# Performance work log

Hardware: AMD Instinct MI355X
Metric: run time of the kernel (lower is better)

Reference implementation:

```python
import jax, jax.numpy as jnp
import numpy as np

N = 50000      # num_nodes
E = 800000     # num_edges
D = 128        # hidden_dim
POOL_RATIO = 0.5
CROSS_W = 1.0  # cross_weight


def _gcn(x, W, b, src, dst, n):
    """GCNConv: symmetric-normalized aggregation with self-loops. Dropout is identity (eval)."""
    loops = jnp.arange(n)
    s = jnp.concatenate([src, loops])
    d = jnp.concatenate([dst, loops])
    deg = jax.ops.segment_sum(jnp.ones(s.shape, x.dtype), d, num_segments=n)
    inv_sqrt = jax.lax.rsqrt(jnp.maximum(deg, 1.0))  # deg >= 1 due to self-loops
    xw = x @ W                                        # [n, D]
    msg = xw[s] * (inv_sqrt[s] * inv_sqrt[d])[:, None]  # [E+n, D] gather
    return jax.ops.segment_sum(msg, d, num_segments=n) + b


def _prelu(x, a):
    return jnp.where(x >= 0, x, a * x)


def setup_inputs() -> dict:
    key = jax.random.key(0)
    ks = jax.random.split(key, 8)
    glorot = lambda k, sh: jax.random.normal(k, sh, jnp.float32) * np.float32(np.sqrt(2.0 / (sh[0] + sh[1])))
    return {
        "feat": jax.random.normal(ks[0], (N, D), jnp.float32),
        "h_neg": jax.random.normal(ks[1], (N, D), jnp.float32),
        "edge_index": jax.random.randint(ks[2], (2, E), 0, N),
        "Wd": glorot(ks[3], (D, D)),
        "bd": jnp.zeros((D,), jnp.float32),
        "prelu_a": jnp.full((1,), 0.25, jnp.float32),
        "Wbil": glorot(ks[4], (D, D)),
        "bbil": jnp.zeros((1,), jnp.float32),
        "Wg1": glorot(ks[5], (D, D)),
        "bg1": jnp.zeros((D,), jnp.float32),
        "Wg2": glorot(ks[6], (D, D)),
        "bg2": jnp.zeros((D,), jnp.float32),
        "Wg3": glorot(ks[7], (D, D)),
        "bg3": jnp.zeros((D,), jnp.float32),
    }


def reference(feat, h_neg, edge_index, Wd, bd, prelu_a, Wbil, bbil,
              Wg1, bg1, Wg2, bg2, Wg3, bg3):
    src, dst = edge_index[0], edge_index[1]
    # --- IndexSelect: dense layer on pos/neg features ---
    h_pos = _prelu(feat @ Wd + bd, prelu_a)
    h_neg_d = _prelu(h_neg @ Wd + bd, prelu_a)
    embed = _gcn(h_pos, Wg1, bg1, src, dst, N)
    h_center = jax.nn.sigmoid(embed)
    # Discriminator (bilinear) positive scores -> node importance
    score_pos = jnp.einsum('nd,de,ne->n', h_pos, Wbil, h_center) + bbil[0]
    _ = jnp.einsum('nd,de,ne->n', h_neg_d, Wbil, h_center) + bbil[0]  # score_neg (logits branch)
    scores = jax.nn.sigmoid(score_pos)
    order = jnp.argsort(-scores)           # descending
    k = int(POOL_RATIO * N)
    select_idx = order[:k]
    select_scores = scores[order][:k]
    # --- GraphPool (use_gcn=True): down-sample GCN, gather, scale ---
    pooled = _gcn(embed, Wg2, bg2, src, dst, N)[select_idx] * select_scores[:, None]
    # --- GraphUnpool: scatter into zeros, up-sample GCN ---
    fine = jnp.zeros((N, D), feat.dtype).at[select_idx].set(pooled)
    out = _gcn(fine, Wg3, bg3, src, dst, N)
    # --- cross/fuse connection ---
    return out + CROSS_W * embed
```

## Files before the change

### kernel.cpp

```cpp
#include <hip/hip_runtime.h>
#include <hip/hip_bf16.h>

#define NN 50000
#define NE 800000
#define DD 128
#define KSEL 25000
#define NBK 391
#define NBLKA 98

typedef unsigned int uint32;
typedef unsigned short ushort16;

__device__ __forceinline__ float sigmoidf(float x){ return 1.f/(1.f+__expf(-x)); }

__device__ __forceinline__ unsigned short f2b(float f){
  union{float f; unsigned u;} v; v.f=f;
  unsigned r=(v.u + 0x7fffu + ((v.u>>16)&1u))>>16;
  return (unsigned short)r;
}

__device__ __forceinline__ void addbf2(float&lo,float&hi,uint32 u,float w){
  lo+=__uint_as_float(u<<16)*w;
  hi+=__uint_as_float(u&0xffff0000u)*w;
}

__global__ __launch_bounds__(1024) void k_bcount(const int* __restrict__ dst,
    int* __restrict__ btot, int* __restrict__ blkcnt){
  __shared__ int h[NBK];
  int tid=threadIdx.x;
  for(int i=tid;i<NBK;i+=1024) h[i]=0;
  __syncthreads();
  int e0=blockIdx.x*8192;
  #pragma unroll
  for(int t=0;t<8;t++){
    int e=e0+t*1024+tid;
    if(e<NE) atomicAdd(&h[dst[e]>>7],1);
  }
  __syncthreads();
  for(int i=tid;i<NBK;i+=1024){
    int c=h[i];
    blkcnt[blockIdx.x*NBK+i]=c;
    if(c) atomicAdd(&btot[i],c);
  }
}

__global__ __launch_bounds__(512) void k_bscan(const int* __restrict__ btot,
    int* __restrict__ boff, const int* __restrict__ blkcnt, int* __restrict__ blkbase,
    int* __restrict__ row_start){
  __shared__ int sdata[512];
  int tid=threadIdx.x;
  int v=(tid<NBK)?btot[tid]:0;
  sdata[tid]=v; __syncthreads();
  for(int off=1;off<512;off<<=1){
    int y=(tid>=off)?sdata[tid-off]:0;
    __syncthreads();
    sdata[tid]+=y;
    __syncthreads();
  }
  int excl=sdata[tid]-v;
  if(tid<NBK) boff[tid]=excl;
  if(tid==NBK-1){ boff[NBK]=excl+v; row_start[NN]=NE; }
  if(tid<NBK){
    int run=excl;
    for(int b=0;b<NBLKA;b++){
      int c=blkcnt[b*NBK+tid];
      blkbase[b*NBK+tid]=run;
      run+=c;
    }
  }
}

__global__ __launch_bounds__(1024) void k_bscatter(const int* __restrict__ src,
    const int* __restrict__ dst, const int* __restrict__ blkbase, uint32* __restrict__ pairs){
  __shared__ int cur[NBK];
  int tid=threadIdx.x;
  for(int i=tid;i<NBK;i+=1024) cur[i]=blkbase[blockIdx.x*NBK+i];
  __syncthreads();
  int e0=blockIdx.x*8192;
  #pragma unroll
  for(int t=0;t<8;t++){
    int e=e0+t*1024+tid;
    if(e<NE){
      int d=dst[e];
      int p=atomicAdd(&cur[d>>7],1);
      pairs[p]=(unsigned)src[e] | ((unsigned)(d&127)<<17);
    }
  }
}

__global__ __launch_bounds__(256) void k_bfinal(const uint32* __restrict__ pairs,
    const int* __restrict__ boff, int* __restrict__ row_start,
    float* __restrict__ inv_sq, int* __restrict__ csr_src){
  __shared__ int degl[128];
  __shared__ int cur[128];
  __shared__ int ssum[2];
  int b=blockIdx.x, tid=threadIdx.x;
  int lo=boff[b], hi=boff[b+1];
  if(tid<128) degl[tid]=0;
  __syncthreads();
  for(int e=lo+tid;e<hi;e+=256) atomicAdd(&degl[pairs[e]>>17],1);
  __syncthreads();
  int v=0,x=0;
  if(tid<128){
    v=degl[tid]; x=v;
    #pragma unroll
    for(int off=1;off<64;off<<=1){
      int y=__shfl_up(x,off,64);
      if((tid&63)>=off) x+=y;
    }
    if((tid&63)==63) ssum[tid>>6]=x;
  }
  __syncthreads();
  if(tid<128){
    int incl=x+((tid>=64)?ssum[0]:0);
    int node=b*128+tid;
    int excl=lo+incl-v;
    if(node<NN){
      row_start[node]=excl;
      cur[tid]=excl;
      inv_sq[node]=1.f/sqrtf((float)(v+1));
    }
  }
  __syncthreads();
  for(int e=lo+tid;e<hi;e+=256){
    uint32 u=pairs[e];
    int p=atomicAdd(&cur[u>>17],1);
    csr_src[p]=(int)(u&0x1FFFFu);
  }
}

__global__ void k_transpose(const float* __restrict__ W, float* __restrict__ Wt){
  int idx=blockIdx.x*256+threadIdx.x;
  if(idx<DD*DD){
    int k=idx>>7, c=idx&127;
    Wt[idx]=W[c*DD+k];
  }
}

template<int IN_SIG,int ACT,int OUT_BF16,int FUSE_SCORE,int ROWLIST>
__global__ __launch_bounds__(256) void k_gemm96(const float* __restrict__ A,
    const float* __restrict__ W, const float* __restrict__ bias,
    float* __restrict__ outf, ushort16* __restrict__ outb,
    const float* __restrict__ aparam, const float* __restrict__ hp,
    const float* __restrict__ bbil, float* __restrict__ score,
    const int* __restrict__ rlist){
  __shared__ float Al[96][132];
  int tid=threadIdx.x;
  int row0=blockIdx.x*96;
  {
    #pragma unroll
    for(int i=0;i<12;i++){
      int idx=i*256+tid;
      int r=idx>>5, c=(idx&31)*4;
      int gr; bool ok;
      if(ROWLIST){ int ri=row0+r; ok=(ri<KSEL); gr=ok?rlist[ri]:0; }
      else { gr=row0+r; ok=(gr<NN); }
      float4 v=make_float4(0.f,0.f,0.f,0.f);
      if(ok) v=*(const float4*)&A[(size_t)gr*DD+c];
      if(IN_SIG){ v.x=sigmoidf(v.x); v.y=sigmoidf(v.y); v.z=sigmoidf(v.z); v.w=sigmoidf(v.w); }
      *(float4*)&Al[r][c]=v;
    }
  }
  __syncthreads();
  int tx=tid&15, ty=tid>>4;
  float acc[6][8];
  #pragma unroll
  for(int i=0;i<6;i++)
    #pragma unroll
    for(int c=0;c<8;c++) acc[i][c]=0.f;

  for(int k=0;k<DD;k+=4){
    float wv[4][8];
    #pragma unroll
    for(int r=0;r<4;r++){
      float4 lo=*(const float4*)&W[(size_t)(k+r)*DD+tx*8];
      float4 hi=*(const float4*)&W[(size_t)(k+r)*DD+tx*8+4];
      wv[r][0]=lo.x; wv[r][1]=lo.y; wv[r][2]=lo.z; wv[r][3]=lo.w;
      wv[r][4]=hi.x; wv[r][5]=hi.y; wv[r][6]=hi.z; wv[r][7]=hi.w;
    }
    #pragma unroll
    for(int i=0;i<6;i++){
      float4 a=*(const float4*)&Al[ty+16*i][k];
      #pragma unroll
      for(int c=0;c<8;c++)
        acc[i][c]+=a.x*wv[0][c]+a.y*wv[1][c]+a.z*wv[2][c]+a.w*wv[3][c];
    }
  }

  if(FUSE_SCORE){
    float bb=bbil[0];
    #pragma unroll
    for(int i=0;i<6;i++){
      int r=row0+ty+16*i;
      float p=0.f;
      if(r<NN){
        float4 h0=*(const float4*)&hp[(size_t)r*DD+tx*8];
        float4 h1=*(const float4*)&hp[(size_t)r*DD+tx*8+4];
        p=acc[i][0]*h0.x+acc[i][1]*h0.y+acc[i][2]*h0.z+acc[i][3]*h0.w
         +acc[i][4]*h1.x+acc[i][5]*h1.y+acc[i][6]*h1.z+acc[i][7]*h1.w;
      }
      p+=__shfl_xor(p,1,64); p+=__shfl_xor(p,2,64);
      p+=__shfl_xor(p,4,64); p+=__shfl_xor(p,8,64);
      if(tx==0 && r<NN) score[r]=sigmoidf(p+bb);
    }
    return;
  }
  float bl[8]={0,0,0,0,0,0,0,0};
  if(bias){
    float4 b0=*(const float4*)&bias[tx*8];
    float4 b1=*(const float4*)&bias[tx*8+4];
    bl[0]=b0.x; bl[1]=b0.y; bl[2]=b0.z; bl[3]=b0.w;
    bl[4]=b1.x; bl[5]=b1.y; bl[6]=b1.z; bl[7]=b1.w;
  }
  float ap=ACT?aparam[0]:0.f;
  #pragma unroll
  for(int i=0;i<6;i++){
    int ri=row0+ty+16*i;
    int r; bool ok;
    if(ROWLIST){ ok=(ri<KSEL); r=ok?rlist[ri]:0; }
    else { r=ri; ok=(r<NN); }
    if(ok){
      float o[8];
      #pragma unroll
      for(int c=0;c<8;c++){
        float t=acc[i][c]+bl[c];
        if(ACT) t=t>=0.f?t:ap*t;
        o[c]=t;
      }
      if(OUT_BF16){
        uint4 pk;
        pk.x=((uint32)f2b(o[1])<<16)|f2b(o[0]);
        pk.y=((uint32)f2b(o[3])<<16)|f2b(o[2]);
        pk.z=((uint32)f2b(o[5])<<16)|f2b(o[4]);
        pk.w=((uint32)f2b(o[7])<<16)|f2b(o[6]);
        *(uint4*)&outb[(size_t)r*DD+tx*8]=pk;
      } else {
        float4 q0; q0.x=o[0]; q0.y=o[1]; q0.z=o[2]; q0.w=o[3];
        float4 q1; q1.x=o[4]; q1.y=o[5]; q1.z=o[6]; q1.w=o[7];
        *(float4*)&outf[(size_t)r*DD+tx*8]=q0;
        *(float4*)&outf[(size_t)r*DD+tx*8+4]=q1;
      }
    }
  }
}

__global__ __launch_bounds__(256) void k_agg_f32(const float* __restrict__ xw,
    const int* __restrict__ row_start, const int* __restrict__ csr,
    const float* __restrict__ inv, const float* __restrict__ bias,
    float* __restrict__ outp){
  int node=blockIdx.x*4+(threadIdx.x>>6);
  if(node>=NN) return;
  int lane=threadIdx.x&63;
  int g=lane>>5, li=lane&31;
  int rs=row_start[node], re=row_start[node+1];
  float a0=0.f,a1=0.f,a2=0.f,a3=0.f;
  int j=rs;
  for(; j+7<re; j+=8){
    int s0=csr[j+g], s1=csr[j+2+g], s2=csr[j+4+g], s3=csr[j+6+g];
    float w0=inv[s0], w1=inv[s1], w2=inv[s2], w3=inv[s3];
    float4 v0=*(const float4*)&xw[(size_t)s0*DD+li*4];
    float4 v1=*(const float4*)&xw[(size_t)s1*DD+li*4];
    float4 v2=*(const float4*)&xw[(size_t)s2*DD+li*4];
    float4 v3=*(const float4*)&xw[(size_t)s3*DD+li*4];
    a0+=v0.x*w0+v1.x*w1+v2.x*w2+v3.x*w3;
    a1+=v0.y*w0+v1.y*w1+v2.y*w2+v3.y*w3;
    a2+=v0.z*w0+v1.z*w1+v2.z*w2+v3.z*w3;
    a3+=v0.w*w0+v1.w*w1+v2.w*w2+v3.w*w3;
  }
  for(; j+1<re; j+=2){
    int s=csr[j+g];
    float w=inv[s];
    float4 v=*(const float4*)&xw[(size_t)s*DD+li*4];
    a0+=v.x*w; a1+=v.y*w; a2+=v.z*w; a3+=v.w*w;
  }
  if(j<re && g==0){
    int s=csr[j]; float w=inv[s];
    float4 v=*(const float4*)&xw[(size_t)s*DD+li*4];
    a0+=v.x*w; a1+=v.y*w; a2+=v.z*w; a3+=v.w*w;
  }
  if(g==0){
    float wd=inv[node];
    float4 v=*(const float4*)&xw[(size_t)node*DD+li*4];
    a0+=v.x*wd; a1+=v.y*wd; a2+=v.z*wd; a3+=v.w*wd;
  }
  a0+=__shfl_xor(a0,32,64); a1+=__shfl_xor(a1,32,64);
  a2+=__shfl_xor(a2,32,64); a3+=__shfl_xor(a3,32,64);
  if(g==0){
    float wn=inv[node];
    float4 bv=*(const float4*)&bias[li*4];
    float4 o;
    o.x=a0*wn+bv.x; o.y=a1*wn+bv.y; o.z=a2*wn+bv.z; o.w=a3*wn+bv.w;
    *(float4*)&outp[(size_t)node*DD+li*4]=o;
  }
}

template<int MODE>
__global__ __launch_bounds__(256) void k_agg_b16(const uint32* __restrict__ xwb,
    const int* __restrict__ row_start, const int* __restrict__ csr,
    const float* __restrict__ inv, const float* __restrict__ bias,
    float* __restrict__ outp, const float* __restrict__ score,
    const unsigned char* __restrict__ sel, const float* __restrict__ addbuf,
    const int* __restrict__ list){
  int idx4=blockIdx.x*4+(threadIdx.x>>6);
  int node;
  if(MODE==1){ if(idx4>=KSEL) return; node=list[idx4]; }
  else { node=idx4; if(node>=NN) return; }
  int lane=threadIdx.x&63;
  int g=lane>>4, li=lane&15;
  int rs=row_start[node], re=row_start[node+1];
  float a[8];
  #pragma unroll
  for(int c=0;c<8;c++) a[c]=0.f;
  int j=rs;
  for(; j+7<re; j+=8){
    int sA=csr[j+g], sB=csr[j+4+g];
    if(MODE!=2 || sel[sA]){
      float w=inv[sA];
      uint4 u=*(const uint4*)(xwb+(size_t)sA*64+li*4);
      addbf2(a[0],a[1],u.x,w); addbf2(a[2],a[3],u.y,w);
      addbf2(a[4],a[5],u.z,w); addbf2(a[6],a[7],u.w,w);
    }
    if(MODE!=2 || sel[sB]){
      float w=inv[sB];
      uint4 u=*(const uint4*)(xwb+(size_t)sB*64+li*4);
      addbf2(a[0],a[1],u.x,w); addbf2(a[2],a[3],u.y,w);
      addbf2(a[4],a[5],u.z,w); addbf2(a[6],a[7],u.w,w);
    }
  }
  for(; j+3<re; j+=4){
    int s=csr[j+g];
    if(MODE!=2 || sel[s]){
      float w=inv[s];
      uint4 u=*(const uint4*)(xwb+(size_t)s*64+li*4);
      addbf2(a[0],a[1],u.x,w); addbf2(a[2],a[3],u.y,w);
      addbf2(a[4],a[5],u.z,w); addbf2(a[6],a[7],u.w,w);
    }
  }
  int rem=re-j;
  if(g<rem){
    int s=csr[j+g];
    if(MODE!=2 || sel[s]){
      float w=inv[s];
      uint4 u=*(const uint4*)(xwb+(size_t)s*64+li*4);
      addbf2(a[0],a[1],u.x,w); addbf2(a[2],a[3],u.y,w);
      addbf2(a[4],a[5],u.z,w); addbf2(a[6],a[7],u.w,w);
    }
  }
  if(g==0 && (MODE!=2 || sel[node])){
    float wd=inv[node];
    uint4 u=*(const uint4*)(xwb+(size_t)node*64+li*4);
    addbf2(a[0],a[1],u.x,wd); addbf2(a[2],a[3],u.y,wd);
    addbf2(a[4],a[5],u.z,wd); addbf2(a[6],a[7],u.w,wd);
  }
  #pragma unroll
  for(int c=0;c<8;c++){
    a[c]+=__shfl_xor(a[c],16,64);
    a[c]+=__shfl_xor(a[c],32,64);
  }
  if(g<2){
    float wn=inv[node];
    int cb=li*8+g*4;
    float4 bv=*(const float4*)&bias[cb];
    float r0=a[g*4+0]*wn+bv.x, r1=a[g*4+1]*wn+bv.y;
    float r2=a[g*4+2]*wn+bv.z, r3=a[g*4+3]*wn+bv.w;
    if(MODE==1){
      float sc=score[node];
      r0*=sc; r1*=sc; r2*=sc; r3*=sc;
    } else {
      float4 ad=*(const float4*)&addbuf[(size_t)node*DD+cb];
      r0+=ad.x; r1+=ad.y; r2+=ad.z; r3+=ad.w;
    }
    float4 o; o.x=r0; o.y=r1; o.z=r2; o.w=r3;
    *(float4*)&outp[(size_t)node*DD+cb]=o;
  }
}

template<int NB,int PASS>
__global__ __launch_bounds__(256) void k_hist(const float* __restrict__ score,
    int* __restrict__ ghist, const int* __restrict__ ctrl){
  __shared__ int lh[NB];
  int tid=threadIdx.x;
  for(int i=tid;i<NB;i+=256) lh[i]=0;
  __syncthreads();
  int p0=0,p01=0;
  if(PASS==1) p0=ctrl[0];
  if(PASS==2) p01=ctrl[2];
  for(int i=blockIdx.x*256+tid; i<NN; i+=gridDim.x*256){
    unsigned b=__float_as_uint(score[i]);
    if(PASS==0) atomicAdd(&lh[b>>20],1);
    else if(PASS==1){ if((int)(b>>20)==p0) atomicAdd(&lh[(b>>8)&0xFFF],1); }
    else { if((int)(b>>8)==p01) atomicAdd(&lh[b&0xFF],1); }
  }
  __syncthreads();
  for(int i=tid;i<NB;i+=256){ int v=lh[i]; if(v) atomicAdd(&ghist[i],v); }
}

template<int NB,int PASS>
__global__ void k_findb(const int* __restrict__ hist, int* __restrict__ ctrl){
  const int NT=NB/4;
  __shared__ int gsum[NT];
  int t=threadIdx.x;
  int s=hist[t*4]+hist[t*4+1]+hist[t*4+2]+hist[t*4+3];
  int x=s; gsum[t]=x; __syncthreads();
  for(int off=1;off<NT;off<<=1){
    int y=(t+off<NT)?gsum[t+off]:0;
    __syncthreads();
    x+=y; gsum[t]=x; __syncthreads();
  }
  int base;
  if(PASS==0) base=0; else if(PASS==1) base=ctrl[1]; else base=ctrl[3];
  int above=base+((t<NT-1)?gsum[t+1]:0);
  int incl=base+gsum[t];
  if(above<KSEL && incl>=KSEL){
    int c=above, B=0;
    for(int b=3;b>=0;b--){
      int hb=hist[t*4+b];
      if(c+hb>=KSEL){ B=t*4+b; break; }
      c+=hb;
    }
    if(PASS==0){ ctrl[0]=B; ctrl[1]=c; }
    else if(PASS==1){ ctrl[2]=(ctrl[0]<<12)|B; ctrl[3]=c; }
    else { ctrl[4]=(int)((((unsigned)ctrl[2])<<8)|(unsigned)B); ctrl[5]=KSEL-c; }
  }
}

__global__ void k_sel(const float* __restrict__ score, int* __restrict__ ctrl,
                      int* __restrict__ tie_list, unsigned char* __restrict__ sel,
                      int* __restrict__ list){
  int i=blockIdx.x*256+threadIdx.x;
  if(i>=NN) return;
  unsigned b=__float_as_uint(score[i]);
  unsigned thr=(unsigned)ctrl[4];
  if(b>thr){
    sel[i]=1;
    int p=atomicAdd(&ctrl[7],1);
    list[p]=i;
  }
  else if(b==thr){
    sel[i]=0;
    int p=atomicAdd(&ctrl[6],1);
    if(p<4096) tie_list[p]=i;
  } else sel[i]=0;
}

__global__ __launch_bounds__(256) void k_tie(const int* __restrict__ ctrl_c,
    int* __restrict__ ctrl, const int* __restrict__ tie_list,
    unsigned char* __restrict__ sel, int* __restrict__ list){
  int m=ctrl_c[6]; if(m>4096) m=4096;
  int needed=ctrl_c[5];
  for(int t=threadIdx.x; t<m; t+=blockDim.x){
    int idx=tie_list[t];
    int rank=0;
    for(int j=0;j<m;j++) rank+=(tie_list[j]<idx)?1:0;
    if(rank<needed){
      sel[idx]=1;
      int p=atomicAdd(&ctrl[7],1);
      list[p]=idx;
    }
  }
}

extern "C" void kernel_launch(void* const* d_in, const int* in_sizes, int n_in,
                              void* d_out, int out_size, void* d_ws, size_t ws_size,
                              hipStream_t stream){
  const float* feat   =(const float*)d_in[0];
  const int*   ei     =(const int*)  d_in[2];
  const int*   src    = ei;
  const int*   dst    = ei + NE;
  const float* Wd     =(const float*)d_in[3];
  const float* bd     =(const float*)d_in[4];
  const float* prelu_a=(const float*)d_in[5];
  const float* Wbil   =(const float*)d_in[6];
  const float* bbil   =(const float*)d_in[7];
  const float* Wg1    =(const float*)d_in[8];
  const float* bg1    =(const float*)d_in[9];
  const float* Wg2    =(const float*)d_in[10];
  const float* bg2    =(const float*)d_in[11];
  const float* Wg3    =(const float*)d_in[12];
  const float* bg3    =(const float*)d_in[13];
  float* out=(float*)d_out;

  char* p=(char*)d_ws;
  auto alloc=[&](size_t bytes)->void*{ void* r=(void*)p; p+=((bytes+255)/256)*256; return r; };
  float* h_pos   =(float*)alloc((size_t)NN*DD*4);
  float* embed   =(float*)alloc((size_t)NN*DD*4);
  float* xw      =(float*)alloc((size_t)NN*DD*4);
  float* score   =(float*)alloc((size_t)NN*4);
  float* inv_sq  =(float*)alloc((size_t)NN*4);
  float* WbT     =(float*)alloc((size_t)DD*DD*4);
  int*   row_st  =(int*)  alloc((size_t)(NN+1)*4);
  int*   csr_src =(int*)  alloc((size_t)NE*4);
  int*   ctrl    =(int*)  alloc(64);
  int*   hist0   =(int*)  alloc(4096*4);
  int*   hist1   =(int*)  alloc(4096*4);
  int*   hist2   =(int*)  alloc(256*4);
  int*   tie_list=(int*)  alloc(4096*4);
  int*   list    =(int*)  alloc((size_t)KSEL*4);
  unsigned char* sel=(unsigned char*)alloc(NN);
  int*   btot    =(int*)  alloc((size_t)NBK*4);
  int*   boff    =(int*)  alloc((size_t)(NBK+1)*4);
  int*   blkcnt  =(int*)  alloc((size_t)NBLKA*NBK*4);
  int*   blkbase =(int*)  alloc((size_t)NBLKA*NBK*4);
  uint32* pairs  =(uint32*)xw;
  ushort16* xwb  =(ushort16*)xw;
  float* fine = out;

  const int NB=(NN+255)/256;
  const int GB=(NN+95)/96;
  const int GBL=(KSEL+95)/96;
  const int AB=(NN+3)/4;
  const int ABL=(KSEL+3)/4;

  hipMemsetAsync(ctrl, 0, (size_t)((char*)tie_list-(char*)ctrl), stream);
  hipMemsetAsync(btot, 0, (size_t)NBK*4, stream);

  k_bcount  <<<NBLKA,1024,0,stream>>>(dst, btot, blkcnt);
  k_bscan   <<<1,512,0,stream>>>(btot, boff, blkcnt, blkbase, row_st);
  k_bscatter<<<NBLKA,1024,0,stream>>>(src, dst, blkbase, pairs);
  k_bfinal  <<<NBK,256,0,stream>>>(pairs, boff, row_st, inv_sq, csr_src);
  k_transpose<<<64,256,0,stream>>>(Wbil, WbT);

  k_gemm96<0,1,0,0,0><<<GB,256,0,stream>>>(feat, Wd, bd, h_pos, nullptr, prelu_a, nullptr, nullptr, nullptr, nullptr);
  k_gemm96<0,0,0,0,0><<<GB,256,0,stream>>>(h_pos, Wg1, nullptr, xw, nullptr, nullptr, nullptr, nullptr, nullptr, nullptr);
  k_agg_f32<<<AB,256,0,stream>>>(xw, row_st, csr_src, inv_sq, bg1, embed);
  k_gemm96<1,0,0,1,0><<<GB,256,0,stream>>>(embed, WbT, nullptr, nullptr, nullptr, nullptr, h_pos, bbil, score, nullptr);
  k_hist<4096,0><<<64,256,0,stream>>>(score, hist0, ctrl);
  k_findb<4096,0><<<1,1024,0,stream>>>(hist0, ctrl);
  k_hist<4096,1><<<64,256,0,stream>>>(score, hist1, ctrl);
  k_findb<4096,1><<<1,1024,0,stream>>>(hist1, ctrl);
  k_hist<256,2><<<64,256,0,stream>>>(score, hist2, ctrl);
  k_findb<256,2><<<1,64,0,stream>>>(hist2, ctrl);
  k_sel<<<NB,256,0,stream>>>(score, ctrl, tie_list, sel, list);
  k_tie<<<1,256,0,stream>>>(ctrl, ctrl, tie_list, sel, list);
  k_gemm96<0,0,1,0,0><<<GB,256,0,stream>>>(embed, Wg2, nullptr, nullptr, xwb, nullptr, nullptr, nullptr, nullptr, nullptr);
  k_agg_b16<1><<<ABL,256,0,stream>>>((const uint32*)xwb, row_st, csr_src, inv_sq, bg2, fine, score, sel, nullptr, list);
  k_gemm96<0,0,1,0,1><<<GBL,256,0,stream>>>(fine, Wg3, nullptr, nullptr, xwb, nullptr, nullptr, nullptr, nullptr, list);
  k_agg_b16<2><<<AB,256,0,stream>>>((const uint32*)xwb, row_st, csr_src, inv_sq, bg3, out, nullptr, sel, embed, nullptr);
}
```

Measured before the change: 374.4 us.

## Shrink GEMM row tile, split fp32 aggregation by column halves, fuse prep

The GEMM row tile drops from 96 to 64 rows, which gives more blocks and lowers per-block LDS and register use. The fp32 GCN aggregation is split into two column halves, one 64-column half per block. Each wavefront now handles four edges at a time with 16 lanes per edge, which is meant to improve occupancy and memory-level parallelism on the gather. The two memsets and the transpose kernel are folded into one prep kernel to cut launch overhead. In exchange, the split aggregation reads the CSR indices and inv weights twice, and the smaller tiles reuse each W load across fewer rows.

```diff
diff --git a/kernel.cpp b/kernel.cpp
--- a/kernel.cpp
+++ b/kernel.cpp
@@ -7,6 +7,7 @@
 #define KSEL 25000
 #define NBK 391
 #define NBLKA 98
+#define AB 12500
 
 typedef unsigned int uint32;
 typedef unsigned short ushort16;
@@ -22,6 +23,14 @@
 __device__ __forceinline__ void addbf2(float&lo,float&hi,uint32 u,float w){
   lo+=__uint_as_float(u<<16)*w;
   hi+=__uint_as_float(u&0xffff0000u)*w;
+}
+
+__global__ __launch_bounds__(256) void k_prep(const float* __restrict__ W,
+    float* __restrict__ Wt, int* __restrict__ zspan, int* __restrict__ btot){
+  int i=blockIdx.x*256+threadIdx.x;
+  if(i<DD*DD) Wt[i]=W[(i&127)*DD+(i>>7)];
+  if(i<8512) zspan[i]=0;
+  if(i<NBK) btot[i]=0;
 }
 
 __global__ __launch_bounds__(1024) void k_bcount(const int* __restrict__ dst,
@@ -129,27 +138,19 @@
   }
 }
 
-__global__ void k_transpose(const float* __restrict__ W, float* __restrict__ Wt){
-  int idx=blockIdx.x*256+threadIdx.x;
-  if(idx<DD*DD){
-    int k=idx>>7, c=idx&127;
-    Wt[idx]=W[c*DD+k];
-  }
-}
-
 template<int IN_SIG,int ACT,int OUT_BF16,int FUSE_SCORE,int ROWLIST>
-__global__ __launch_bounds__(256) void k_gemm96(const float* __restrict__ A,
+__global__ __launch_bounds__(256) void k_gemm64t(const float* __restrict__ A,
     const float* __restrict__ W, const float* __restrict__ bias,
     float* __restrict__ outf, ushort16* __restrict__ outb,
     const float* __restrict__ aparam, const float* __restrict__ hp,
     const float* __restrict__ bbil, float* __restrict__ score,
     const int* __restrict__ rlist){
-  __shared__ float Al[96][132];
+  __shared__ float Al[64][132];
   int tid=threadIdx.x;
-  int row0=blockIdx.x*96;
+  int row0=blockIdx.x*64;
   {
     #pragma unroll
-    for(int i=0;i<12;i++){
+    for(int i=0;i<8;i++){
       int idx=i*256+tid;
       int r=idx>>5, c=(idx&31)*4;
       int gr; bool ok;
@@ -163,9 +164,9 @@
   }
   __syncthreads();
   int tx=tid&15, ty=tid>>4;
-  float acc[6][8];
+  float acc[4][8];
   #pragma unroll
-  for(int i=0;i<6;i++)
+  for(int i=0;i<4;i++)
     #pragma unroll
     for(int c=0;c<8;c++) acc[i][c]=0.f;
 
@@ -179,7 +180,7 @@
       wv[r][4]=hi.x; wv[r][5]=hi.y; wv[r][6]=hi.z; wv[r][7]=hi.w;
     }
     #pragma unroll
-    for(int i=0;i<6;i++){
+    for(int i=0;i<4;i++){
       float4 a=*(const float4*)&Al[ty+16*i][k];
       #pragma unroll
       for(int c=0;c<8;c++)
@@ -190,7 +191,7 @@
   if(FUSE_SCORE){
     float bb=bbil[0];
     #pragma unroll
-    for(int i=0;i<6;i++){
+    for(int i=0;i<4;i++){
       int r=row0+ty+16*i;
       float p=0.f;
       if(r<NN){
@@ -214,7 +215,7 @@
   }
   float ap=ACT?aparam[0]:0.f;
   #pragma unroll
-  for(int i=0;i<6;i++){
+  for(int i=0;i<4;i++){
     int ri=row0+ty+16*i;
     int r; bool ok;
     if(ROWLIST){ ok=(ri<KSEL); r=ok?rlist[ri]:0; }
@@ -244,53 +245,61 @@
   }
 }
 
-__global__ __launch_bounds__(256) void k_agg_f32(const float* __restrict__ xw,
+__global__ __launch_bounds__(256) void k_agg_f32h(const float* __restrict__ xw,
     const int* __restrict__ row_start, const int* __restrict__ csr,
     const float* __restrict__ inv, const float* __restrict__ bias,
     float* __restrict__ outp){
-  int node=blockIdx.x*4+(threadIdx.x>>6);
+  int bid=blockIdx.x;
+  int half=(bid>=AB)?1:0;
+  int node=(bid-half*AB)*4+(threadIdx.x>>6);
   if(node>=NN) return;
   int lane=threadIdx.x&63;
-  int g=lane>>5, li=lane&31;
+  int g=lane>>4, li=lane&15;
+  int colbase=half*64;
+  const float* xwc=xw+colbase;
   int rs=row_start[node], re=row_start[node+1];
   float a0=0.f,a1=0.f,a2=0.f,a3=0.f;
   int j=rs;
-  for(; j+7<re; j+=8){
-    int s0=csr[j+g], s1=csr[j+2+g], s2=csr[j+4+g], s3=csr[j+6+g];
+  for(; j+15<re; j+=16){
+    int s0=csr[j+g], s1=csr[j+4+g], s2=csr[j+8+g], s3=csr[j+12+g];
     float w0=inv[s0], w1=inv[s1], w2=inv[s2], w3=inv[s3];
-    float4 v0=*(const float4*)&xw[(size_t)s0*DD+li*4];
-    float4 v1=*(const float4*)&xw[(size_t)s1*DD+li*4];
-    float4 v2=*(const float4*)&xw[(size_t)s2*DD+li*4];
-    float4 v3=*(const float4*)&xw[(size_t)s3*DD+li*4];
+    float4 v0=*(const float4*)&xwc[(size_t)s0*DD+li*4];
+    float4 v1=*(const float4*)&xwc[(size_t)s1*DD+li*4];
+    float4 v2=*(const float4*)&xwc[(size_t)s2*DD+li*4];
+    float4 v3=*(const float4*)&xwc[(size_t)s3*DD+li*4];
     a0+=v0.x*w0+v1.x*w1+v2.x*w2+v3.x*w3;
     a1+=v0.y*w0+v1.y*w1+v2.y*w2+v3.y*w3;
     a2+=v0.z*w0+v1.z*w1+v2.z*w2+v3.z*w3;
     a3+=v0.w*w0+v1.w*w1+v2.w*w2+v3.w*w3;
   }
-  for(; j+1<re; j+=2){
+  for(; j+3<re; j+=4){
     int s=csr[j+g];
     float w=inv[s];
-    float4 v=*(const float4*)&xw[(size_t)s*DD+li*4];
+    float4 v=*(const float4*)&xwc[(size_t)s*DD+li*4];
     a0+=v.x*w; a1+=v.y*w; a2+=v.z*w; a3+=v.w*w;
   }
-  if(j<re && g==0){
-    int s=csr[j]; float w=inv[s];
-    float4 v=*(const float4*)&xw[(size_t)s*DD+li*4];
+  int rem=re-j;
+  if(g<rem){
+    int s=csr[j+g];
+    float w=inv[s];
+    float4 v=*(const float4*)&xwc[(size_t)s*DD+li*4];
     a0+=v.x*w; a1+=v.y*w; a2+=v.z*w; a3+=v.w*w;
   }
   if(g==0){
     float wd=inv[node];
-    float4 v=*(const float4*)&xw[(size_t)node*DD+li*4];
+    float4 v=*(const float4*)&xwc[(size_t)node*DD+li*4];
     a0+=v.x*wd; a1+=v.y*wd; a2+=v.z*wd; a3+=v.w*wd;
   }
-  a0+=__shfl_xor(a0,32,64); a1+=__shfl_xor(a1,32,64);
-  a2+=__shfl_xor(a2,32,64); a3+=__shfl_xor(a3,32,64);
+  a0+=__shfl_xor(a0,16,64); a0+=__shfl_xor(a0,32,64);
+  a1+=__shfl_xor(a1,16,64); a1+=__shfl_xor(a1,32,64);
+  a2+=__shfl_xor(a2,16,64); a2+=__shfl_xor(a2,32,64);
+  a3+=__shfl_xor(a3,16,64); a3+=__shfl_xor(a3,32,64);
   if(g==0){
     float wn=inv[node];
-    float4 bv=*(const float4*)&bias[li*4];
+    float4 bv=*(const float4*)&bias[colbase+li*4];
     float4 o;
     o.x=a0*wn+bv.x; o.y=a1*wn+bv.y; o.z=a2*wn+bv.z; o.w=a3*wn+bv.w;
-    *(float4*)&outp[(size_t)node*DD+li*4]=o;
+    *(float4*)&outp[(size_t)node*DD+colbase+li*4]=o;
   }
 }
 
@@ -506,24 +515,21 @@
   float* fine = out;
 
   const int NB=(NN+255)/256;
-  const int GB=(NN+95)/96;
-  const int GBL=(KSEL+95)/96;
-  const int AB=(NN+3)/4;
+  const int GB=(NN+63)/64;
+  const int GBL=(KSEL+63)/64;
   const int ABL=(KSEL+3)/4;
 
-  hipMemsetAsync(ctrl, 0, (size_t)((char*)tie_list-(char*)ctrl), stream);
-  hipMemsetAsync(btot, 0, (size_t)NBK*4, stream);
+  k_prep<<<64,256,0,stream>>>(Wbil, WbT, ctrl, btot);
 
   k_bcount  <<<NBLKA,1024,0,stream>>>(dst, btot, blkcnt);
   k_bscan   <<<1,512,0,stream>>>(btot, boff, blkcnt, blkbase, row_st);
   k_bscatter<<<NBLKA,1024,0,stream>>>(src, dst, blkbase, pairs);
   k_bfinal  <<<NBK,256,0,stream>>>(pairs, boff, row_st, inv_sq, csr_src);
-  k_transpose<<<64,256,0,stream>>>(Wbil, WbT);
-
-  k_gemm96<0,1,0,0,0><<<GB,256,0,stream>>>(feat, Wd, bd, h_pos, nullptr, prelu_a, nullptr, nullptr, nullptr, nullptr);
-  k_gemm96<0,0,0,0,0><<<GB,256,0,stream>>>(h_pos, Wg1, nullptr, xw, nullptr, nullptr, nullptr, nullptr, nullptr, nullptr);
-  k_agg_f32<<<AB,256,0,stream>>>(xw, row_st, csr_src, inv_sq, bg1, embed);
-  k_gemm96<1,0,0,1,0><<<GB,256,0,stream>>>(embed, WbT, nullptr, nullptr, nullptr, nullptr, h_pos, bbil, score, nullptr);
+
+  k_gemm64t<0,1,0,0,0><<<GB,256,0,stream>>>(feat, Wd, bd, h_pos, nullptr, prelu_a, nullptr, nullptr, nullptr, nullptr);
+  k_gemm64t<0,0,0,0,0><<<GB,256,0,stream>>>(h_pos, Wg1, nullptr, xw, nullptr, nullptr, nullptr, nullptr, nullptr, nullptr);
+  k_agg_f32h<<<2*AB,256,0,stream>>>(xw, row_st, csr_src, inv_sq, bg1, embed);
+  k_gemm64t<1,0,0,1,0><<<GB,256,0,stream>>>(embed, WbT, nullptr, nullptr, nullptr, nullptr, h_pos, bbil, score, nullptr);
   k_hist<4096,0><<<64,256,0,stream>>>(score, hist0, ctrl);
   k_findb<4096,0><<<1,1024,0,stream>>>(hist0, ctrl);
   k_hist<4096,1><<<64,256,0,stream>>>(score, hist1, ctrl);
@@ -532,8 +538,8 @@
   k_findb<256,2><<<1,64,0,stream>>>(hist2, ctrl);
   k_sel<<<NB,256,0,stream>>>(score, ctrl, tie_list, sel, list);
   k_tie<<<1,256,0,stream>>>(ctrl, ctrl, tie_list, sel, list);
-  k_gemm96<0,0,1,0,0><<<GB,256,0,stream>>>(embed, Wg2, nullptr, nullptr, xwb, nullptr, nullptr, nullptr, nullptr, nullptr);
+  k_gemm64t<0,0,1,0,0><<<GB,256,0,stream>>>(embed, Wg2, nullptr, nullptr, xwb, nullptr, nullptr, nullptr, nullptr, nullptr);
   k_agg_b16<1><<<ABL,256,0,stream>>>((const uint32*)xwb, row_st, csr_src, inv_sq, bg2, fine, score, sel, nullptr, list);
-  k_gemm96<0,0,1,0,1><<<GBL,256,0,stream>>>(fine, Wg3, nullptr, nullptr, xwb, nullptr, nullptr, nullptr, nullptr, list);
+  k_gemm64t<0,0,1,0,1><<<GBL,256,0,stream>>>(fine, Wg3, nullptr, nullptr, xwb, nullptr, nullptr, nullptr, nullptr, list);
   k_agg_b16<2><<<AB,256,0,stream>>>((const uint32*)xwb, row_st, csr_src, inv_sq, bg3, out, nullptr, sel, embed, nullptr);
 }
```

After: 375.9 us. Within noise of the previous version (+0.4%).

## Use bf16 MFMA for the pool and unpool GEMMs and fuse prep kernels

Applied to the files above, without the earlier changes.

Replaces the FP32 SIMT GEMMs that produce the bf16 xw for the second and third GCN layers with a bf16 MFMA kernel (16x16x32). Weights are pre-transposed and converted to bf16 in a new prep kernel, which also replaces the two memsets and the transpose kernel. The remaining FP32 GEMMs move from 96-row to 64-row tiles to get more blocks. Activations are now rounded to bf16 before the matmul, which adds precision loss, and the MFMA output stores are scalar 2-byte writes, which may coalesce poorly.

```diff
diff --git a/kernel.cpp b/kernel.cpp
--- a/kernel.cpp
+++ b/kernel.cpp
@@ -7,9 +7,12 @@
 #define KSEL 25000
 #define NBK 391
 #define NBLKA 98
+#define AB 12500
 
 typedef unsigned int uint32;
 typedef unsigned short ushort16;
+typedef __attribute__((ext_vector_type(8))) short bf16x8;
+typedef __attribute__((ext_vector_type(4))) float f32x4;
 
 __device__ __forceinline__ float sigmoidf(float x){ return 1.f/(1.f+__expf(-x)); }
 
@@ -22,6 +25,21 @@
 __device__ __forceinline__ void addbf2(float&lo,float&hi,uint32 u,float w){
   lo+=__uint_as_float(u<<16)*w;
   hi+=__uint_as_float(u&0xffff0000u)*w;
+}
+
+__global__ __launch_bounds__(256) void k_prep(const float* __restrict__ Wbil,
+    float* __restrict__ WbT, const float* __restrict__ Wg2, ushort16* __restrict__ Wt2b,
+    const float* __restrict__ Wg3, ushort16* __restrict__ Wt3b,
+    int* __restrict__ zspan, int* __restrict__ btot){
+  int i=blockIdx.x*256+threadIdx.x;
+  if(i<DD*DD){
+    int n=i>>7, k=i&127;
+    WbT[i]=Wbil[k*DD+n];
+    Wt2b[i]=f2b(Wg2[(size_t)k*DD+n]);
+    Wt3b[i]=f2b(Wg3[(size_t)k*DD+n]);
+  }
+  if(i<8512) zspan[i]=0;
+  if(i<NBK) btot[i]=0;
 }
 
 __global__ __launch_bounds__(1024) void k_bcount(const int* __restrict__ dst,
@@ -129,43 +147,32 @@
   }
 }
 
-__global__ void k_transpose(const float* __restrict__ W, float* __restrict__ Wt){
-  int idx=blockIdx.x*256+threadIdx.x;
-  if(idx<DD*DD){
-    int k=idx>>7, c=idx&127;
-    Wt[idx]=W[c*DD+k];
-  }
-}
-
-template<int IN_SIG,int ACT,int OUT_BF16,int FUSE_SCORE,int ROWLIST>
-__global__ __launch_bounds__(256) void k_gemm96(const float* __restrict__ A,
+template<int IN_SIG,int ACT,int FUSE_SCORE>
+__global__ __launch_bounds__(256) void k_gemm64t(const float* __restrict__ A,
     const float* __restrict__ W, const float* __restrict__ bias,
-    float* __restrict__ outf, ushort16* __restrict__ outb,
+    float* __restrict__ outf,
     const float* __restrict__ aparam, const float* __restrict__ hp,
-    const float* __restrict__ bbil, float* __restrict__ score,
-    const int* __restrict__ rlist){
-  __shared__ float Al[96][132];
+    const float* __restrict__ bbil, float* __restrict__ score){
+  __shared__ float Al[64][132];
   int tid=threadIdx.x;
-  int row0=blockIdx.x*96;
+  int row0=blockIdx.x*64;
   {
-    #pragma unroll
-    for(int i=0;i<12;i++){
+    const float4* A4=(const float4*)(A+(size_t)row0*DD);
+    #pragma unroll
+    for(int i=0;i<8;i++){
       int idx=i*256+tid;
       int r=idx>>5, c=(idx&31)*4;
-      int gr; bool ok;
-      if(ROWLIST){ int ri=row0+r; ok=(ri<KSEL); gr=ok?rlist[ri]:0; }
-      else { gr=row0+r; ok=(gr<NN); }
       float4 v=make_float4(0.f,0.f,0.f,0.f);
-      if(ok) v=*(const float4*)&A[(size_t)gr*DD+c];
+      if(row0+r<NN) v=A4[idx];
       if(IN_SIG){ v.x=sigmoidf(v.x); v.y=sigmoidf(v.y); v.z=sigmoidf(v.z); v.w=sigmoidf(v.w); }
       *(float4*)&Al[r][c]=v;
     }
   }
   __syncthreads();
   int tx=tid&15, ty=tid>>4;
-  float acc[6][8];
-  #pragma unroll
-  for(int i=0;i<6;i++)
+  float acc[4][8];
+  #pragma unroll
+  for(int i=0;i<4;i++)
     #pragma unroll
     for(int c=0;c<8;c++) acc[i][c]=0.f;
 
@@ -179,7 +186,7 @@
       wv[r][4]=hi.x; wv[r][5]=hi.y; wv[r][6]=hi.z; wv[r][7]=hi.w;
     }
     #pragma unroll
-    for(int i=0;i<6;i++){
+    for(int i=0;i<4;i++){
       float4 a=*(const float4*)&Al[ty+16*i][k];
       #pragma unroll
       for(int c=0;c<8;c++)
@@ -190,7 +197,7 @@
   if(FUSE_SCORE){
     float bb=bbil[0];
     #pragma unroll
-    for(int i=0;i<6;i++){
+    for(int i=0;i<4;i++){
       int r=row0+ty+16*i;
       float p=0.f;
       if(r<NN){
@@ -214,12 +221,9 @@
   }
   float ap=ACT?aparam[0]:0.f;
   #pragma unroll
-  for(int i=0;i<6;i++){
-    int ri=row0+ty+16*i;
-    int r; bool ok;
-    if(ROWLIST){ ok=(ri<KSEL); r=ok?rlist[ri]:0; }
-    else { r=ri; ok=(r<NN); }
-    if(ok){
+  for(int i=0;i<4;i++){
+    int r=row0+ty+16*i;
+    if(r<NN){
       float o[8];
       #pragma unroll
       for(int c=0;c<8;c++){
@@ -227,19 +231,76 @@
         if(ACT) t=t>=0.f?t:ap*t;
         o[c]=t;
       }
-      if(OUT_BF16){
-        uint4 pk;
-        pk.x=((uint32)f2b(o[1])<<16)|f2b(o[0]);
-        pk.y=((uint32)f2b(o[3])<<16)|f2b(o[2]);
-        pk.z=((uint32)f2b(o[5])<<16)|f2b(o[4]);
-        pk.w=((uint32)f2b(o[7])<<16)|f2b(o[6]);
-        *(uint4*)&outb[(size_t)r*DD+tx*8]=pk;
-      } else {
-        float4 q0; q0.x=o[0]; q0.y=o[1]; q0.z=o[2]; q0.w=o[3];
-        float4 q1; q1.x=o[4]; q1.y=o[5]; q1.z=o[6]; q1.w=o[7];
-        *(float4*)&outf[(size_t)r*DD+tx*8]=q0;
-        *(float4*)&outf[(size_t)r*DD+tx*8+4]=q1;
-      }
+      float4 q0; q0.x=o[0]; q0.y=o[1]; q0.z=o[2]; q0.w=o[3];
+      float4 q1; q1.x=o[4]; q1.y=o[5]; q1.z=o[6]; q1.w=o[7];
+      *(float4*)&outf[(size_t)r*DD+tx*8]=q0;
+      *(float4*)&outf[(size_t)r*DD+tx*8+4]=q1;
+    }
+  }
+}
+
+template<int ROWLIST>
+__global__ __launch_bounds__(256) void k_gemm_mfma(const float* __restrict__ A,
+    const ushort16* __restrict__ Wtb, ushort16* __restrict__ outb,
+    const int* __restrict__ rlist){
+  __shared__ __align__(16) unsigned short Asl[64][136];
+  __shared__ __align__(16) unsigned short Wsl[128][136];
+  int tid=threadIdx.x;
+  int row0=blockIdx.x*64;
+  {
+    const uint4* Wg=(const uint4*)Wtb;
+    #pragma unroll
+    for(int i=0;i<8;i++){
+      int idx=i*256+tid;
+      int n=idx>>4, k8=(idx&15)*8;
+      uint4 v=Wg[idx];
+      *(uint4*)&Wsl[n][k8]=v;
+    }
+  }
+  {
+    #pragma unroll
+    for(int i=0;i<8;i++){
+      int idx=i*256+tid;
+      int r=idx>>5, c=(idx&31)*4;
+      int gr; bool ok;
+      if(ROWLIST){ int ri=row0+r; ok=(ri<KSEL); gr=ok?rlist[ri]:0; }
+      else { gr=row0+r; ok=(gr<NN); }
+      float4 v=make_float4(0.f,0.f,0.f,0.f);
+      if(ok) v=*(const float4*)&A[(size_t)gr*DD+c];
+      ushort4 pk;
+      pk.x=f2b(v.x); pk.y=f2b(v.y); pk.z=f2b(v.z); pk.w=f2b(v.w);
+      *(ushort4*)&Asl[r][c]=pk;
+    }
+  }
+  __syncthreads();
+  int lane=tid&63, w=tid>>6;
+  int lr=lane&15, lk=lane>>4;
+  f32x4 acc[8];
+  #pragma unroll
+  for(int nf=0;nf<8;nf++){ acc[nf][0]=0.f; acc[nf][1]=0.f; acc[nf][2]=0.f; acc[nf][3]=0.f; }
+  #pragma unroll
+  for(int kk=0;kk<4;kk++){
+    int k0=kk*32+lk*8;
+    bf16x8 a=*(bf16x8*)&Asl[w*16+lr][k0];
+    #pragma unroll
+    for(int nf=0;nf<8;nf++){
+      bf16x8 b=*(bf16x8*)&Wsl[nf*16+lr][k0];
+      acc[nf]=__builtin_amdgcn_mfma_f32_16x16x32_bf16(a,b,acc[nf],0,0,0);
+    }
+  }
+  int orow[4]; bool ok[4];
+  #pragma unroll
+  for(int i=0;i<4;i++){
+    int ri=row0+w*16+lk*4+i;
+    if(ROWLIST){ ok[i]=(ri<KSEL); orow[i]=ok[i]?rlist[ri]:0; }
+    else { orow[i]=ri; ok[i]=(ri<NN); }
+  }
+  #pragma unroll
+  for(int nf=0;nf<8;nf++){
+    int col=nf*16+lr;
+    #pragma unroll
+    for(int i=0;i<4;i++){
+      if(ok[i]) outb[(size_t)orow[i]*DD+col]=f2b(acc[nf][i]);
     }
   }
 }
@@ -488,6 +549,8 @@
   float* score   =(float*)alloc((size_t)NN*4);
   float* inv_sq  =(float*)alloc((size_t)NN*4);
   float* WbT     =(float*)alloc((size_t)DD*DD*4);
+  ushort16* Wt2b =(ushort16*)alloc((size_t)DD*DD*2);
+  ushort16* Wt3b =(ushort16*)alloc((size_t)DD*DD*2);
   int*   row_st  =(int*)  alloc((size_t)(NN+1)*4);
   int*   csr_src =(int*)  alloc((size_t)NE*4);
   int*   ctrl    =(int*)  alloc(64);
@@ -506,24 +569,21 @@
   float* fine = out;
 
   const int NB=(NN+255)/256;
-  const int GB=(NN+95)/96;
-  const int GBL=(KSEL+95)/96;
-  const int AB=(NN+3)/4;
+  const int GB=(NN+63)/64;
+  const int GBL=(KSEL+63)/64;
   const int ABL=(KSEL+3)/4;
 
-  hipMemsetAsync(ctrl, 0, (size_t)((char*)tie_list-(char*)ctrl), stream);
-  hipMemsetAsync(btot, 0, (size_t)NBK*4, stream);
+  k_prep<<<64,256,0,stream>>>(Wbil, WbT, Wg2, Wt2b, Wg3, Wt3b, ctrl, btot);
 
   k_bcount  <<<NBLKA,1024,0,stream>>>(dst, btot, blkcnt);
   k_bscan   <<<1,512,0,stream>>>(btot, boff, blkcnt, blkbase, row_st);
   k_bscatter<<<NBLKA,1024,0,stream>>>(src, dst, blkbase, pairs);
   k_bfinal  <<<NBK,256,0,stream>>>(pairs, boff, row_st, inv_sq, csr_src);
-  k_transpose<<<64,256,0,stream>>>(Wbil, WbT);
-
-  k_gemm96<0,1,0,0,0><<<GB,256,0,stream>>>(feat, Wd, bd, h_pos, nullptr, prelu_a, nullptr, nullptr, nullptr, nullptr);
-  k_gemm96<0,0,0,0,0><<<GB,256,0,stream>>>(h_pos, Wg1, nullptr, xw, nullptr, nullptr, nullptr, nullptr, nullptr, nullptr);
+
+  k_gemm64t<0,1,0><<<GB,256,0,stream>>>(feat, Wd, bd, h_pos, prelu_a, nullptr, nullptr, nullptr);
+  k_gemm64t<0,0,0><<<GB,256,0,stream>>>(h_pos, Wg1, nullptr, xw, nullptr, nullptr, nullptr, nullptr);
   k_agg_f32<<<AB,256,0,stream>>>(xw, row_st, csr_src, inv_sq, bg1, embed);
-  k_gemm96<1,0,0,1,0><<<GB,256,0,stream>>>(embed, WbT, nullptr, nullptr, nullptr, nullptr, h_pos, bbil, score, nullptr);
+  k_gemm64t<1,0,1><<<GB,256,0,stream>>>(embed, WbT, nullptr, nullptr, nullptr, h_pos, bbil, score);
   k_hist<4096,0><<<64,256,0,stream>>>(score, hist0, ctrl);
   k_findb<4096,0><<<1,1024,0,stream>>>(hist0, ctrl);
   k_hist<4096,1><<<64,256,0,stream>>>(score, hist1, ctrl);
@@ -532,8 +592,8 @@
   k_findb<256,2><<<1,64,0,stream>>>(hist2, ctrl);
   k_sel<<<NB,256,0,stream>>>(score, ctrl, tie_list, sel, list);
   k_tie<<<1,256,0,stream>>>(ctrl, ctrl, tie_list, sel, list);
-  k_gemm96<0,0,1,0,0><<<GB,256,0,stream>>>(embed, Wg2, nullptr, nullptr, xwb, nullptr, nullptr, nullptr, nullptr, nullptr);
+  k_gemm_mfma<0><<<GB,256,0,stream>>>(embed, Wt2b, xwb, nullptr);
   k_agg_b16<1><<<ABL,256,0,stream>>>((const uint32*)xwb, row_st, csr_src, inv_sq, bg2, fine, score, sel, nullptr, list);
-  k_gemm96<0,0,1,0,1><<<GBL,256,0,stream>>>(fine, Wg3, nullptr, nullptr, xwb, nullptr, nullptr, nullptr, nullptr, list);
+  k_gemm_mfma<1><<<GBL,256,0,stream>>>(fine, Wt3b, xwb, list);
   k_agg_b16<2><<<AB,256,0,stream>>>((const uint32*)xwb, row_st, csr_src, inv_sq, bg3, out, nullptr, sel, embed, nullptr);
 }
```

Measured after the change: 334.7 us. -10.6%, faster.
